# Performance work log

Measured on AMD Instinct MI355X. Metric: run time of the kernel, lower is better.

## Reference

```python
import jax, jax.numpy as jnp
import numpy as np

BATCH, N_SEQS, SEQ_LEN, D_IN, D_OUT = 8, 4, 2048, 512, 512
LN_EPS = 1e-5


def setup_inputs() -> dict:
    key = jax.random.key(0)
    ks = jax.random.split(key, 6)
    s_in = 1.0 / np.sqrt(D_IN)
    s_out = 1.0 / np.sqrt(D_OUT)
    return {
        "x": jax.random.normal(ks[0], (BATCH, N_SEQS * SEQ_LEN * D_IN), dtype=jnp.float32),
        "Wq": jax.random.normal(ks[1], (D_OUT, D_IN), dtype=jnp.float32) * s_in,
        "Wk": jax.random.normal(ks[2], (D_OUT, D_IN), dtype=jnp.float32) * s_in,
        "Wv": jax.random.normal(ks[3], (D_OUT, D_IN), dtype=jnp.float32) * s_in,
        "Wo": jax.random.normal(ks[4], (D_OUT, D_OUT), dtype=jnp.float32) * s_out,
        "bo": jnp.zeros((D_OUT,), dtype=jnp.float32),
        "gamma": jnp.ones((D_OUT,), dtype=jnp.float32),
        "beta": jnp.zeros((D_OUT,), dtype=jnp.float32),
    }


def _phi(x):
    # positive feature map: elu(x) + 1
    return jax.nn.elu(x) + 1.0


def reference(x, Wq, Wk, Wv, Wo, bo, gamma, beta):
    batch = x.shape[0]
    xs = x.reshape(batch * N_SEQS, SEQ_LEN, D_IN)  # [B*L, S, d_in]
    Q = _phi(jnp.einsum('bsi,oi->bso', xs, Wq))     # [B*L, S, d_out]
    K = _phi(jnp.einsum('bsi,oi->bso', xs, Wk))
    V = jnp.einsum('bsi,oi->bso', xs, Wv)
    kv = jnp.einsum('bsd,bse->bde', K, V)           # [B*L, d_out, d_out]
    num = jnp.einsum('bsd,bde->bse', Q, kv)         # [B*L, S, d_out]
    k_sum = K.sum(axis=1, keepdims=True)            # [B*L, 1, d_out]
    den = jnp.maximum((Q * k_sum).sum(axis=-1, keepdims=True), 1e-6)
    out = num / den
    y = jnp.einsum('bse,oe->bso', out, Wo) + bo + out  # out_proj + residual
    mu = y.mean(axis=-1, keepdims=True)
    var = ((y - mu) ** 2).mean(axis=-1, keepdims=True)
    y = (y - mu) * jax.lax.rsqrt(var + LN_EPS) * gamma + beta
    return y.reshape(batch, -1)
```

## Files before the change

kernel.cpp:

```cpp
#include <hip/hip_runtime.h>
#include <cstdint>

typedef __bf16 bf16x8 __attribute__((ext_vector_type(8)));
typedef float  f32x4  __attribute__((ext_vector_type(4)));

#define SEQS   32
#define SLEN   2048
#define DIM    512
#define MROWS  65536

static __device__ __forceinline__ void load_lds16(const void* g, void* l) {
  __builtin_amdgcn_global_load_lds(
      (const __attribute__((address_space(1))) void*)(uintptr_t)g,
      (__attribute__((address_space(3))) void*)(uintptr_t)l,
      16, 0, 0);
}

static __device__ __forceinline__ unsigned short bfbits(float f) {
  __bf16 h = (__bf16)f;
  unsigned short u;
  __builtin_memcpy(&u, &h, 2);
  return u;
}

static __device__ __forceinline__ void gemm_core(
    const __bf16* __restrict__ A, int lda, int arow0,
    const __bf16* __restrict__ B, int ldb, int brow0,
    int K, __bf16* Asm, __bf16* Bsm, f32x4 (&acc)[4][4])
{
  const int tid  = threadIdx.x;
  const int wave = tid >> 6;
  const int lane = tid & 63;
  const int wr = wave >> 1, wc = wave & 1;
  const int lr = lane & 15, kq = lane >> 4;

  for (int kt = 0; kt < K; kt += 64) {
#pragma unroll
    for (int q = 0; q < 4; ++q) {
      const int L  = q * 4096 + tid * 16;
      const int r  = L >> 7;
      const int sl = (L >> 4) & 7;
      const int c  = ((sl ^ (r & 7)) << 3);
      load_lds16(A + (size_t)(arow0 + r) * lda + (kt + c),
                 (char*)Asm + q * 4096 + wave * 1024);
      load_lds16(B + (size_t)(brow0 + r) * ldb + (kt + c),
                 (char*)Bsm + q * 4096 + wave * 1024);
    }
    __syncthreads();

    bf16x8 af[2][4], bfr[2][4];
#pragma unroll
    for (int kk = 0; kk < 2; ++kk)
#pragma unroll
      for (int i = 0; i < 4; ++i) {
        const int rA = wr * 64 + i * 16 + lr;
        af[kk][i] = *reinterpret_cast<const bf16x8*>(
            (char*)Asm + rA * 128 + ((((kk * 4 + kq) ^ (rA & 7))) << 4));
        const int rB = wc * 64 + i * 16 + lr;
        bfr[kk][i] = *reinterpret_cast<const bf16x8*>(
            (char*)Bsm + rB * 128 + ((((kk * 4 + kq) ^ (rB & 7))) << 4));
      }
#pragma unroll
    for (int kk = 0; kk < 2; ++kk)
#pragma unroll
      for (int i = 0; i < 4; ++i)
#pragma unroll
        for (int j = 0; j < 4; ++j)
          acc[i][j] = __builtin_amdgcn_mfma_f32_16x16x32_bf16(
              af[kk][i], bfr[kk][j], acc[i][j], 0, 0, 0);
    __syncthreads();
  }
}


__global__ __launch_bounds__(256) void cast_kernel(
    const float* __restrict__ src, __bf16* __restrict__ dst, int n8)
{
  int i = blockIdx.x * blockDim.x + threadIdx.x;
  const int stride = gridDim.x * blockDim.x;
  for (; i < n8; i += stride) {
    const float4* p = reinterpret_cast<const float4*>(src + (size_t)i * 8);
    float4 a = p[0], b2 = p[1];
    float vals[8] = {a.x, a.y, a.z, a.w, b2.x, b2.y, b2.z, b2.w};
    uint32_t w[4];
#pragma unroll
    for (int t = 0; t < 4; ++t)
      w[t] = (uint32_t)bfbits(vals[2 * t]) | ((uint32_t)bfbits(vals[2 * t + 1]) << 16);
    uint4 o; o.x = w[0]; o.y = w[1]; o.z = w[2]; o.w = w[3];
    *reinterpret_cast<uint4*>(dst + (size_t)i * 8) = o;
  }
}

__global__ __launch_bounds__(256) void cast4_kernel(
    const float* __restrict__ a, const float* __restrict__ b,
    const float* __restrict__ c, const float* __restrict__ d,
    __bf16* __restrict__ ab, __bf16* __restrict__ bb,
    __bf16* __restrict__ cb, __bf16* __restrict__ db)
{
  const int z = blockIdx.y;
  const float* src = (z == 0) ? a : (z == 1) ? b : (z == 2) ? c : d;
  __bf16* dst = (z == 0) ? ab : (z == 1) ? bb : (z == 2) ? cb : db;
  const int i = blockIdx.x * 256 + threadIdx.x;
  const float4* p = reinterpret_cast<const float4*>(src + (size_t)i * 8);
  float4 x = p[0], y = p[1];
  float vals[8] = {x.x, x.y, x.z, x.w, y.x, y.y, y.z, y.w};
  uint32_t w[4];
#pragma unroll
  for (int t = 0; t < 4; ++t)
    w[t] = (uint32_t)bfbits(vals[2 * t]) | ((uint32_t)bfbits(vals[2 * t + 1]) << 16);
  uint4 o; o.x = w[0]; o.y = w[1]; o.z = w[2]; o.w = w[3];
  *reinterpret_cast<uint4*>(dst + (size_t)i * 8) = o;
}

__global__ __launch_bounds__(512, 1) void qkv_kernel(
    const __bf16* __restrict__ xb,
    const __bf16* __restrict__ Wqb, const __bf16* __restrict__ Wkb,
    const __bf16* __restrict__ Wvb,
    __bf16* __restrict__ Q, __bf16* __restrict__ KT, __bf16* __restrict__ VT,
    float* __restrict__ ksum)
{
  __shared__ __align__(16) __bf16 As[2][256 * 64];
  __shared__ __align__(16) __bf16 Bs[2][256 * 64];
  const int b = blockIdx.x;
  const int xcd = b & 7, loc = b >> 3;
  const int brow = (loc / 6) * 8 + xcd;
  const int inner = loc % 6;
  const int z = inner >> 1, bcol = inner & 1;
  const __bf16* W = (z == 0) ? Wqb : (z == 1) ? Wkb : Wvb;

  const int tid = threadIdx.x, wave = tid >> 6, lane = tid & 63;
  const int wr = wave >> 2, wn = wave & 3;
  const int lr = lane & 15, kq = lane >> 4;

  const __bf16* Abase = xb + (size_t)(brow * 256) * DIM;
  const __bf16* Bbase = W + (size_t)(bcol * 256) * DIM;

  auto stage = [&](int s, int kt) {
#pragma unroll
    for (int q = 0; q < 4; ++q) {
      const int L  = q * 8192 + tid * 16;
      const int r  = L >> 7;
      const int sl = (L >> 4) & 7;
      const int c  = ((sl ^ (r & 7)) << 3);
      load_lds16(Abase + (size_t)r * DIM + (kt + c),
                 (char*)(&As[s][0]) + q * 8192 + wave * 1024);
      load_lds16(Bbase + (size_t)r * DIM + (kt + c),
                 (char*)(&Bs[s][0]) + q * 8192 + wave * 1024);
    }
  };

  f32x4 acc[8][4] = {};

  stage(0, 0);
  __syncthreads();
  for (int t = 0; t < 8; ++t) {
    const int cur = t & 1;
    if (t < 7) stage(cur ^ 1, (t + 1) * 64);
#pragma unroll
    for (int kk = 0; kk < 2; ++kk) {
      bf16x8 bfr[4], af[8];
#pragma unroll
      for (int j = 0; j < 4; ++j) {
        const int rB = wn * 64 + j * 16 + lr;
        bfr[j] = *reinterpret_cast<const bf16x8*>(
            (const char*)(&Bs[cur][0]) + rB * 128 + (((kk * 4 + kq) ^ (rB & 7)) << 4));
      }
#pragma unroll
      for (int i = 0; i < 8; ++i) {
        const int rA = wr * 128 + i * 16 + lr;
        af[i] = *reinterpret_cast<const bf16x8*>(
            (const char*)(&As[cur][0]) + rA * 128 + (((kk * 4 + kq) ^ (rA & 7)) << 4));
      }
#pragma unroll
      for (int i = 0; i < 8; ++i)
#pragma unroll
        for (int j = 0; j < 4; ++j)
          acc[i][j] = __builtin_amdgcn_mfma_f32_16x16x32_bf16(af[i], bfr[j], acc[i][j], 0, 0, 0);
    }
    __syncthreads();
  }

  const int m00 = brow * 256 + wr * 128 + kq * 4;
  const int n00 = bcol * 256 + wn * 64 + lr;
  if (z == 0) {
#pragma unroll
    for (int i = 0; i < 8; ++i)
#pragma unroll
      for (int j = 0; j < 4; ++j) {
        const int n = n00 + j * 16;
#pragma unroll
        for (int r = 0; r < 4; ++r) {
          const int m = m00 + i * 16 + r;
          float v = acc[i][j][r];
          v = (v > 0.f) ? (v + 1.f) : __expf(v);
          Q[(size_t)m * DIM + n] = (__bf16)v;
        }
      }
  } else {
    __bf16* T = (z == 1) ? KT : VT;
    const int seq = (brow * 256) >> 11;
    float ks[4] = {0.f, 0.f, 0.f, 0.f};
#pragma unroll
    for (int i = 0; i < 8; ++i) {
      const int mb = m00 + i * 16;
      const int s0 = mb & 2047;
#pragma unroll
      for (int j = 0; j < 4; ++j) {
        const int d = n00 + j * 16;
        unsigned short h[4];
#pragma unroll
        for (int r = 0; r < 4; ++r) {
          float v = acc[i][j][r];
          if (z == 1) { v = (v > 0.f) ? (v + 1.f) : __expf(v); ks[j] += v; }
          h[r] = bfbits(v);
        }
        uint2 u;
        u.x = (uint32_t)h[0] | ((uint32_t)h[1] << 16);
        u.y = (uint32_t)h[2] | ((uint32_t)h[3] << 16);
        *reinterpret_cast<uint2*>(T + ((size_t)(seq * DIM + d) << 11) + s0) = u;
      }
    }
    if (z == 1) {
#pragma unroll
      for (int j = 0; j < 4; ++j) {
        float p = ks[j];
        p += __shfl_xor(p, 16, 64);
        p += __shfl_xor(p, 32, 64);
        if (kq == 0) atomicAdd(&ksum[seq * DIM + n00 + j * 16], p);
      }
    }
  }
}

__global__ __launch_bounds__(256) void den_kernel(
    const __bf16* __restrict__ Q, const float* __restrict__ ksum,
    float* __restrict__ den)
{
  const int lane = threadIdx.x & 63;
  const int m = blockIdx.x * 4 + (threadIdx.x >> 6);
  bf16x8 qv = *reinterpret_cast<const bf16x8*>(Q + (size_t)m * DIM + lane * 8);
  const float* kp = ksum + ((m >> 11) << 9) + lane * 8;
  float s = 0.f;
#pragma unroll
  for (int t = 0; t < 8; ++t) s += (float)qv[t] * kp[t];
#pragma unroll
  for (int off = 32; off > 0; off >>= 1) s += __shfl_xor(s, off, 64);
  if (lane == 0) den[m] = fmaxf(s, 1e-6f);
}

__global__ __launch_bounds__(256) void kv_kernel(
    const __bf16* __restrict__ VT, const __bf16* __restrict__ KT,
    __bf16* __restrict__ kvT)
{
  __shared__ __align__(16) __bf16 Asm[128 * 64];
  __shared__ __align__(16) __bf16 Bsm[128 * 64];
  const int b = blockIdx.x;
  const int xcd = b & 7, loc = b >> 3;
  const int seq = (loc >> 4) * 8 + xcd;
  const int inner = loc & 15;
  const int bxx = inner >> 2, byy = inner & 3;
  const __bf16* A = VT + (size_t)seq * DIM * SLEN;
  const __bf16* B = KT + (size_t)seq * DIM * SLEN;
  f32x4 acc[4][4] = {};
  gemm_core(A, SLEN, bxx * 128, B, SLEN, byy * 128, SLEN, Asm, Bsm, acc);

  const int tid = threadIdx.x, wave = tid >> 6, lane = tid & 63;
  const int wr = wave >> 1, wc = wave & 1, lr = lane & 15, kq = lane >> 4;
  const int m0 = bxx * 128 + wr * 64 + kq * 4;
  const int n0 = byy * 128 + wc * 64 + lr;
  __bf16* C = kvT + (size_t)seq * DIM * DIM;
#pragma unroll
  for (int i = 0; i < 4; ++i)
#pragma unroll
    for (int j = 0; j < 4; ++j)
#pragma unroll
      for (int r = 0; r < 4; ++r)
        C[(size_t)(m0 + i * 16 + r) * DIM + (n0 + j * 16)] = (__bf16)acc[i][j][r];
}

__global__ __launch_bounds__(256) void num_kernel(
    const __bf16* __restrict__ Q, const __bf16* __restrict__ kvT,
    const float* __restrict__ den, __bf16* __restrict__ out)
{
  __shared__ __align__(16) __bf16 Asm[128 * 64];
  __shared__ __align__(16) __bf16 Bsm[128 * 64];
  const int b = blockIdx.x;
  const int xcd = b & 7, loc = b >> 3;
  const int seq = (loc >> 6) * 8 + xcd;
  const int inner = loc & 63;
  const int brow = seq * 16 + (inner >> 2);
  const int bcol = inner & 3;
  f32x4 acc[4][4] = {};
  gemm_core(Q, DIM, brow * 128, kvT + (size_t)seq * DIM * DIM, DIM,
            bcol * 128, DIM, Asm, Bsm, acc);

  const int tid = threadIdx.x, wave = tid >> 6, lane = tid & 63;
  const int wr = wave >> 1, wc = wave & 1, lr = lane & 15, kq = lane >> 4;
  const int m0 = brow * 128 + wr * 64 + kq * 4;
  const int n0 = bcol * 128 + wc * 64 + lr;
  float rden[4][4];
#pragma unroll
  for (int i = 0; i < 4; ++i)
#pragma unroll
    for (int r = 0; r < 4; ++r)
      rden[i][r] = 1.f / den[m0 + i * 16 + r];
#pragma unroll
  for (int i = 0; i < 4; ++i)
#pragma unroll
    for (int j = 0; j < 4; ++j)
#pragma unroll
      for (int r = 0; r < 4; ++r)
        out[(size_t)(m0 + i * 16 + r) * DIM + (n0 + j * 16)] =
            (__bf16)(acc[i][j][r] * rden[i][r]);
}

__global__ __launch_bounds__(512, 1) void final_kernel(
    const __bf16* __restrict__ outb, const __bf16* __restrict__ Wob,
    const float* __restrict__ bo, const float* __restrict__ gamma,
    const float* __restrict__ beta, float* __restrict__ y)
{
  __shared__ __align__(16) __bf16 Asm[2][128 * 32];
  __shared__ __align__(16) __bf16 Bsm[2][512 * 32];
  __shared__ float redS[2][128], redSS[2][128];
  const int tid = threadIdx.x, wave = tid >> 6, lane = tid & 63;
  const int Wr = wave >> 1, Wc = wave & 1;
  const int lr = lane & 15, kq = lane >> 4;
  const int brow = blockIdx.x;
  f32x4 acc[2][16] = {};

  auto stage = [&](int s, int kt) {
    {
      const int L = tid * 16;
      const int r = L >> 6, sl = (L >> 4) & 3;
      const int c = ((sl ^ ((r >> 1) & 3)) << 3);
      load_lds16(outb + (size_t)(brow * 128 + r) * DIM + (kt + c),
                 (char*)(&Asm[s][0]) + wave * 1024);
    }
#pragma unroll
    for (int q = 0; q < 4; ++q) {
      const int L = q * 8192 + tid * 16;
      const int r = L >> 6, sl = (L >> 4) & 3;
      const int c = ((sl ^ ((r >> 1) & 3)) << 3);
      load_lds16(Wob + (size_t)r * DIM + (kt + c),
                 (char*)(&Bsm[s][0]) + q * 8192 + wave * 1024);
    }
  };

  stage(0, 0);
  __syncthreads();
  for (int t = 0; t < 16; ++t) {
    const int cur = t & 1;
    if (t < 15) stage(cur ^ 1, (t + 1) * 32);
    bf16x8 af[2];
#pragma unroll
    for (int i = 0; i < 2; ++i) {
      const int rA = Wr * 32 + i * 16 + lr;
      af[i] = *reinterpret_cast<const bf16x8*>(
          (char*)(&Asm[cur][0]) + rA * 64 + ((kq ^ ((rA >> 1) & 3)) << 4));
    }
#pragma unroll
    for (int j = 0; j < 16; ++j) {
      const int rB = Wc * 256 + j * 16 + lr;
      bf16x8 bf = *reinterpret_cast<const bf16x8*>(
          (char*)(&Bsm[cur][0]) + rB * 64 + ((kq ^ ((rB >> 1) & 3)) << 4));
#pragma unroll
      for (int i = 0; i < 2; ++i)
        acc[i][j] = __builtin_amdgcn_mfma_f32_16x16x32_bf16(af[i], bf, acc[i][j], 0, 0, 0);
    }
    __syncthreads();
  }

  const int m0g = brow * 128;
  float sA[2][4] = {{0.f}}, ssA[2][4] = {{0.f}};
#pragma unroll
  for (int j = 0; j < 16; ++j) {
    const int n = Wc * 256 + j * 16 + lr;
    const float bon = bo[n];
#pragma unroll
    for (int i = 0; i < 2; ++i) {
      const int mb = m0g + Wr * 32 + i * 16 + kq * 4;
#pragma unroll
      for (int r = 0; r < 4; ++r) {
        float v = acc[i][j][r] + bon + (float)outb[(size_t)(mb + r) * DIM + n];
        acc[i][j][r] = v;
        sA[i][r] += v; ssA[i][r] += v * v;
      }
    }
  }
#pragma unroll
  for (int i = 0; i < 2; ++i)
#pragma unroll
    for (int r = 0; r < 4; ++r) {
      float s = sA[i][r], ss = ssA[i][r];
#pragma unroll
      for (int off = 1; off <= 8; off <<= 1) {
        s  += __shfl_xor(s,  off, 64);
        ss += __shfl_xor(ss, off, 64);
      }
      if (lr == 0) {
        const int ml = Wr * 32 + i * 16 + kq * 4 + r;
        redS[Wc][ml] = s; redSS[Wc][ml] = ss;
      }
    }
  __syncthreads();
  float mu_[2][4], rs_[2][4];
#pragma unroll
  for (int i = 0; i < 2; ++i)
#pragma unroll
    for (int r = 0; r < 4; ++r) {
      const int ml = Wr * 32 + i * 16 + kq * 4 + r;
      const float S  = redS[0][ml]  + redS[1][ml];
      const float SS = redSS[0][ml] + redSS[1][ml];
      const float mu = S * (1.f / 512.f);
      const float var = SS * (1.f / 512.f) - mu * mu;
      mu_[i][r] = mu;
      rs_[i][r] = rsqrtf(var + 1e-5f);
    }
#pragma unroll
  for (int j = 0; j < 16; ++j) {
    const int n = Wc * 256 + j * 16 + lr;
    const float g = gamma[n], bb = beta[n];
#pragma unroll
    for (int i = 0; i < 2; ++i) {
      const int mb = m0g + Wr * 32 + i * 16 + kq * 4;
#pragma unroll
      for (int r = 0; r < 4; ++r)
        y[(size_t)(mb + r) * DIM + n] = (acc[i][j][r] - mu_[i][r]) * rs_[i][r] * g + bb;
    }
  }
}

extern "C" void kernel_launch(void* const* d_in, const int* in_sizes, int n_in,
                              void* d_out, int out_size, void* d_ws, size_t ws_size,
                              hipStream_t stream)
{
  const float* x     = (const float*)d_in[0];
  const float* Wq    = (const float*)d_in[1];
  const float* Wk    = (const float*)d_in[2];
  const float* Wv    = (const float*)d_in[3];
  const float* Wo    = (const float*)d_in[4];
  const float* bo    = (const float*)d_in[5];
  const float* gamma = (const float*)d_in[6];
  const float* beta  = (const float*)d_in[7];
  float* outp = (float*)d_out;

  char* ws = (char*)d_ws;
  const size_t SZ = 67108864;
  __bf16* xb   = (__bf16*)(ws + 0);
  __bf16* Q    = (__bf16*)(ws + SZ);
  __bf16* KT   = (__bf16*)(ws + 2 * SZ);
  __bf16* VT   = (__bf16*)(ws + 3 * SZ);
  __bf16* kvT  = (__bf16*)(ws + 4 * SZ);
  __bf16* Wqb  = (__bf16*)(ws + 4 * SZ + 16777216);
  __bf16* Wkb  = Wqb + 262144;
  __bf16* Wvb  = Wkb + 262144;
  __bf16* Wob  = Wvb + 262144;
  float*  ksum = (float*)(Wob + 262144);
  float*  den  = (float*)((char*)ksum + 65536);

  hipMemsetAsync(ksum, 0, SEQS * DIM * sizeof(float), stream);
  cast_kernel<<<4096, 256, 0, stream>>>(x, xb, MROWS * DIM / 8);
  cast4_kernel<<<dim3(128, 4), 256, 0, stream>>>(Wq, Wk, Wv, Wo, Wqb, Wkb, Wvb, Wob);

  qkv_kernel<<<1536, 512, 0, stream>>>(xb, Wqb, Wkb, Wvb, Q, KT, VT, ksum);
  den_kernel<<<16384, 256, 0, stream>>>(Q, ksum, den);
  kv_kernel<<<512, 256, 0, stream>>>(VT, KT, kvT);
  num_kernel<<<2048, 256, 0, stream>>>(Q, kvT, den, xb );
  final_kernel<<<512, 512, 0, stream>>>(xb, Wob, bo, gamma, beta, outp);
}
```

Before: 398.9 us.

## Enlarge num_kernel tiles to 256x256 and rebalance final_kernel wave layout

num_kernel moves from 128x128 tiles on 256 threads to 256x256 tiles on 512 threads, with its own double-buffered, XOR-swizzled LDS pipeline and vectorized den loads. Grid drops from 2048 to 512 blocks. This raises arithmetic intensity and cuts redundant Q/kv loads. final_kernel changes its wave grid from 4x2 to 2x4 so each wave holds a 4x8 fragment set, improving A/B fragment reuse, with a 4-way LayerNorm reduction. The cost is higher register pressure, 128KB of LDS, and fewer blocks per GPU, which may hurt occupancy.

```diff
diff --git a/kernel.cpp b/kernel.cpp
--- a/kernel.cpp
+++ b/kernel.cpp
@@ -278,40 +278,84 @@
         C[(size_t)(m0 + i * 16 + r) * DIM + (n0 + j * 16)] = (__bf16)acc[i][j][r];
 }
 
-__global__ __launch_bounds__(256) void num_kernel(
+__global__ __launch_bounds__(512, 1) void num_kernel(
     const __bf16* __restrict__ Q, const __bf16* __restrict__ kvT,
     const float* __restrict__ den, __bf16* __restrict__ out)
 {
-  __shared__ __align__(16) __bf16 Asm[128 * 64];
-  __shared__ __align__(16) __bf16 Bsm[128 * 64];
+  __shared__ __align__(16) __bf16 As[2][256 * 64];
+  __shared__ __align__(16) __bf16 Bs[2][256 * 64];
   const int b = blockIdx.x;
   const int xcd = b & 7, loc = b >> 3;
-  const int seq = (loc >> 6) * 8 + xcd;
-  const int inner = loc & 63;
-  const int brow = seq * 16 + (inner >> 2);
-  const int bcol = inner & 3;
-  f32x4 acc[4][4] = {};
-  gemm_core(Q, DIM, brow * 128, kvT + (size_t)seq * DIM * DIM, DIM,
-            bcol * 128, DIM, Asm, Bsm, acc);
+  const int seq = (loc >> 4) * 8 + xcd;
+  const int inner = loc & 15;
+  const int brow = inner >> 1, bcol = inner & 1;
+  const size_t grow0 = (size_t)seq * SLEN + brow * 256;
 
   const int tid = threadIdx.x, wave = tid >> 6, lane = tid & 63;
-  const int wr = wave >> 1, wc = wave & 1, lr = lane & 15, kq = lane >> 4;
-  const int m0 = brow * 128 + wr * 64 + kq * 4;
-  const int n0 = bcol * 128 + wc * 64 + lr;
-  float rden[4][4];
-#pragma unroll
-  for (int i = 0; i < 4; ++i)
-#pragma unroll
-    for (int r = 0; r < 4; ++r)
-      rden[i][r] = 1.f / den[m0 + i * 16 + r];
-#pragma unroll
-  for (int i = 0; i < 4; ++i)
+  const int wr = wave >> 2, wn = wave & 3;
+  const int lr = lane & 15, kq = lane >> 4;
+
+  const __bf16* Abase = Q + grow0 * DIM;
+  const __bf16* Bbase = kvT + (size_t)seq * DIM * DIM + (size_t)(bcol * 256) * DIM;
+
+  auto stage = [&](int s, int kt) {
+#pragma unroll
+    for (int q = 0; q < 4; ++q) {
+      const int L  = q * 8192 + tid * 16;
+      const int r  = L >> 7;
+      const int sl = (L >> 4) & 7;
+      const int c  = ((sl ^ (r & 7)) << 3);
+      load_lds16(Abase + (size_t)r * DIM + (kt + c),
+                 (char*)(&As[s][0]) + q * 8192 + wave * 1024);
+      load_lds16(Bbase + (size_t)r * DIM + (kt + c),
+                 (char*)(&Bs[s][0]) + q * 8192 + wave * 1024);
+    }
+  };
+
+  f32x4 acc[8][4] = {};
+
+  stage(0, 0);
+  __syncthreads();
+  for (int t = 0; t < 8; ++t) {
+    const int cur = t & 1;
+    if (t < 7) stage(cur ^ 1, (t + 1) * 64);
+#pragma unroll
+    for (int kk = 0; kk < 2; ++kk) {
+      bf16x8 bfr[4], af[8];
+#pragma unroll
+      for (int j = 0; j < 4; ++j) {
+        const int rB = wn * 64 + j * 16 + lr;
+        bfr[j] = *reinterpret_cast<const bf16x8*>(
+            (const char*)(&Bs[cur][0]) + rB * 128 + (((kk * 4 + kq) ^ (rB & 7)) << 4));
+      }
+#pragma unroll
+      for (int i = 0; i < 8; ++i) {
+        const int rA = wr * 128 + i * 16 + lr;
+        af[i] = *reinterpret_cast<const bf16x8*>(
+            (const char*)(&As[cur][0]) + rA * 128 + (((kk * 4 + kq) ^ (rA & 7)) << 4));
+      }
+#pragma unroll
+      for (int i = 0; i < 8; ++i)
+#pragma unroll
+        for (int j = 0; j < 4; ++j)
+          acc[i][j] = __builtin_amdgcn_mfma_f32_16x16x32_bf16(af[i], bfr[j], acc[i][j], 0, 0, 0);
+    }
+    __syncthreads();
+  }
+
+  const size_t g0 = grow0 + wr * 128 + kq * 4;
+  const int n00 = bcol * 256 + wn * 64 + lr;
+#pragma unroll
+  for (int i = 0; i < 8; ++i) {
+    const float4 dv = *reinterpret_cast<const float4*>(den + g0 + i * 16);
+    const float rd[4] = {1.f / dv.x, 1.f / dv.y, 1.f / dv.z, 1.f / dv.w};
 #pragma unroll
     for (int j = 0; j < 4; ++j)
 #pragma unroll
       for (int r = 0; r < 4; ++r)
-        out[(size_t)(m0 + i * 16 + r) * DIM + (n0 + j * 16)] =
-            (__bf16)(acc[i][j][r] * rden[i][r]);
+        out[(g0 + i * 16 + r) * DIM + (n00 + j * 16)] =
+            (__bf16)(acc[i][j][r] * rd[r]);
+  }
 }
 
 __global__ __launch_bounds__(512, 1) void final_kernel(
@@ -321,12 +365,12 @@
 {
   __shared__ __align__(16) __bf16 Asm[2][128 * 32];
   __shared__ __align__(16) __bf16 Bsm[2][512 * 32];
-  __shared__ float redS[2][128], redSS[2][128];
+  __shared__ float redS[4][128], redSS[4][128];
   const int tid = threadIdx.x, wave = tid >> 6, lane = tid & 63;
-  const int Wr = wave >> 1, Wc = wave & 1;
+  const int Wr = wave >> 2, Wc = wave & 3;
   const int lr = lane & 15, kq = lane >> 4;
   const int brow = blockIdx.x;
-  f32x4 acc[2][16] = {};
+  f32x4 acc[4][8] = {};
 
   auto stage = [&](int s, int kt) {
     {
@@ -351,34 +395,34 @@
   for (int t = 0; t < 16; ++t) {
     const int cur = t & 1;
     if (t < 15) stage(cur ^ 1, (t + 1) * 32);
-    bf16x8 af[2];
-#pragma unroll
-    for (int i = 0; i < 2; ++i) {
-      const int rA = Wr * 32 + i * 16 + lr;
+    bf16x8 af[4];
+#pragma unroll
+    for (int i = 0; i < 4; ++i) {
+      const int rA = Wr * 64 + i * 16 + lr;
       af[i] = *reinterpret_cast<const bf16x8*>(
           (char*)(&Asm[cur][0]) + rA * 64 + ((kq ^ ((rA >> 1) & 3)) << 4));
     }
 #pragma unroll
-    for (int j = 0; j < 16; ++j) {
-      const int rB = Wc * 256 + j * 16 + lr;
+    for (int j = 0; j < 8; ++j) {
+      const int rB = Wc * 128 + j * 16 + lr;
       bf16x8 bf = *reinterpret_cast<const bf16x8*>(
           (char*)(&Bsm[cur][0]) + rB * 64 + ((kq ^ ((rB >> 1) & 3)) << 4));
 #pragma unroll
-      for (int i = 0; i < 2; ++i)
+      for (int i = 0; i < 4; ++i)
         acc[i][j] = __builtin_amdgcn_mfma_f32_16x16x32_bf16(af[i], bf, acc[i][j], 0, 0, 0);
     }
     __syncthreads();
   }
 
   const int m0g = brow * 128;
-  float sA[2][4] = {{0.f}}, ssA[2][4] = {{0.f}};
-#pragma unroll
-  for (int j = 0; j < 16; ++j) {
-    const int n = Wc * 256 + j * 16 + lr;
+  float sA[4][4] = {{0.f}}, ssA[4][4] = {{0.f}};
+#pragma unroll
+  for (int j = 0; j < 8; ++j) {
+    const int n = Wc * 128 + j * 16 + lr;
     const float bon = bo[n];
 #pragma unroll
-    for (int i = 0; i < 2; ++i) {
-      const int mb = m0g + Wr * 32 + i * 16 + kq * 4;
+    for (int i = 0; i < 4; ++i) {
+      const int mb = m0g + Wr * 64 + i * 16 + kq * 4;
 #pragma unroll
       for (int r = 0; r < 4; ++r) {
         float v = acc[i][j][r] + bon + (float)outb[(size_t)(mb + r) * DIM + n];
@@ -388,7 +432,7 @@
     }
   }
 #pragma unroll
-  for (int i = 0; i < 2; ++i)
+  for (int i = 0; i < 4; ++i)
 #pragma unroll
     for (int r = 0; r < 4; ++r) {
       float s = sA[i][r], ss = ssA[i][r];
@@ -398,31 +442,31 @@
         ss += __shfl_xor(ss, off, 64);
       }
       if (lr == 0) {
-        const int ml = Wr * 32 + i * 16 + kq * 4 + r;
+        const int ml = Wr * 64 + i * 16 + kq * 4 + r;
         redS[Wc][ml] = s; redSS[Wc][ml] = ss;
       }
     }
   __syncthreads();
-  float mu_[2][4], rs_[2][4];
-#pragma unroll
-  for (int i = 0; i < 2; ++i)
+  float mu_[4][4], rs_[4][4];
+#pragma unroll
+  for (int i = 0; i < 4; ++i)
 #pragma unroll
     for (int r = 0; r < 4; ++r) {
-      const int ml = Wr * 32 + i * 16 + kq * 4 + r;
-      const float S  = redS[0][ml]  + redS[1][ml];
-      const float SS = redSS[0][ml] + redSS[1][ml];
+      const int ml = Wr * 64 + i * 16 + kq * 4 + r;
+      const float S  = redS[0][ml] + redS[1][ml] + redS[2][ml] + redS[3][ml];
+      const float SS = redSS[0][ml] + redSS[1][ml] + redSS[2][ml] + redSS[3][ml];
       const float mu = S * (1.f / 512.f);
       const float var = SS * (1.f / 512.f) - mu * mu;
       mu_[i][r] = mu;
       rs_[i][r] = rsqrtf(var + 1e-5f);
     }
 #pragma unroll
-  for (int j = 0; j < 16; ++j) {
-    const int n = Wc * 256 + j * 16 + lr;
+  for (int j = 0; j < 8; ++j) {
+    const int n = Wc * 128 + j * 16 + lr;
     const float g = gamma[n], bb = beta[n];
 #pragma unroll
-    for (int i = 0; i < 2; ++i) {
-      const int mb = m0g + Wr * 32 + i * 16 + kq * 4;
+    for (int i = 0; i < 4; ++i) {
+      const int mb = m0g + Wr * 64 + i * 16 + kq * 4;
 #pragma unroll
       for (int r = 0; r < 4; ++r)
         y[(size_t)(mb + r) * DIM + n] = (acc[i][j][r] - mu_[i][r]) * rs_[i][r] * g + bb;
@@ -465,6 +509,6 @@
   qkv_kernel<<<1536, 512, 0, stream>>>(xb, Wqb, Wkb, Wvb, Q, KT, VT, ksum);
   den_kernel<<<16384, 256, 0, stream>>>(Q, ksum, den);
   kv_kernel<<<512, 256, 0, stream>>>(VT, KT, kvT);
-  num_kernel<<<2048, 256, 0, stream>>>(Q, kvT, den, xb );
+  num_kernel<<<512, 512, 0, stream>>>(Q, kvT, den, xb );
   final_kernel<<<512, 512, 0, stream>>>(xb, Wob, bo, gamma, beta, outp);
 }
```

Measured after the change: 393.4 us. Within noise of the previous version (-1.4%).
